# Performance work log

Hardware: AMD Instinct MI355X
Metric: run time of the kernel (lower is better)

## Reference

```python
import jax, jax.numpy as jnp
from jax import lax
import numpy as np

DIM = 256
D_INNER = 2 * DIM
STATE = 64
NUM_LAYERS = 2
NUM_STACKS = 4  # 0=h_fwd, 1=h_bwd, 2=v_fwd, 3=v_bwd
SPATIAL_H = 32
SPATIAL_W = 64
EPS = 1e-5


def setup_inputs() -> dict:
    key = jax.random.key(0)
    ks = jax.random.split(key, 24)
    w = lambda k, shape: jax.random.normal(k, shape, jnp.float32) * 0.02
    B = 4
    N = SPATIAL_H * SPATIAL_W
    inp = {
        "stream_sem": jax.random.normal(ks[0], (B, N, DIM), jnp.float32),
        "stream_inst": jax.random.normal(ks[1], (B, N, DIM), jnp.float32),
        # per-stack, per-layer Mamba params
        "Wx": w(ks[2], (NUM_STACKS, NUM_LAYERS, DIM, D_INNER)),
        "Wz": w(ks[3], (NUM_STACKS, NUM_LAYERS, DIM, D_INNER)),
        "Wdt": w(ks[4], (NUM_STACKS, NUM_LAYERS, DIM, D_INNER)),
        "WB": w(ks[5], (NUM_STACKS, NUM_LAYERS, DIM, STATE)),
        "WC": w(ks[6], (NUM_STACKS, NUM_LAYERS, DIM, STATE)),
        "A_log": jax.random.normal(ks[7], (NUM_STACKS, NUM_LAYERS, D_INNER), jnp.float32) * 0.1,
        "Dskip": jnp.ones((NUM_STACKS, NUM_LAYERS, D_INNER), jnp.float32),
        "dt_bias": w(ks[8], (NUM_STACKS, NUM_LAYERS, D_INNER)),
        "Wout": w(ks[9], (NUM_STACKS, NUM_LAYERS, D_INNER, DIM)),
        "ln_s": jnp.ones((NUM_STACKS, NUM_LAYERS, DIM), jnp.float32),
        "ln_b": jnp.zeros((NUM_STACKS, NUM_LAYERS, DIM), jnp.float32),
        # merge gates for the two DirectionalBiCMS (0=horizontal, 1=vertical)
        "gate_W": w(ks[10], (2, 2 * DIM, DIM)),
        "gate_b": jnp.zeros((2, DIM), jnp.float32),
        # final sem/inst merges (Linear + LayerNorm); 0=sem, 1=inst
        "merge_W": w(ks[11], (2, 2 * DIM, DIM)),
        "merge_b": jnp.zeros((2, DIM), jnp.float32),
        "merge_ln_s": jnp.ones((2, DIM), jnp.float32),
        "merge_ln_b": jnp.zeros((2, DIM), jnp.float32),
    }
    return inp


def _layernorm(x, s, b):
    mu = jnp.mean(x, axis=-1, keepdims=True)
    xc = x - mu
    var = jnp.mean(xc * xc, axis=-1, keepdims=True)
    return xc * lax.rsqrt(var + EPS) * s + b


def _mamba_layer(x, Wx, Wz, Wdt, WB, WC, A_log, Dskip, dt_bias, Wout, ln_s, ln_b):
    # x: (Bs, L, DIM)
    h = _layernorm(x, ln_s, ln_b)
    xin = h @ Wx                                   # (Bs, L, D_INNER)
    z = h @ Wz
    dt = jax.nn.softplus(h @ Wdt + dt_bias)        # (Bs, L, D_INNER)
    Bm = h @ WB                                    # (Bs, L, STATE)
    Cm = h @ WC
    xs = jax.nn.silu(xin)
    A = -jnp.exp(A_log)                            # (D_INNER,)

    def step(hs, ins):
        dt_t, x_t, B_t, C_t = ins                  # (Bs,Di),(Bs,Di),(Bs,S),(Bs,S)
        hs = jnp.exp(dt_t * A)[..., None] * hs + (dt_t * x_t)[..., None] * B_t[:, None, :]
        y = jnp.einsum('bds,bs->bd', hs, C_t)
        return hs, y

    Bsz = x.shape[0]
    h0 = jnp.zeros((Bsz, Wx.shape[1], WB.shape[1]), x.dtype)
    mv = lambda a: jnp.moveaxis(a, 1, 0)
    _, yT = lax.scan(step, h0, (mv(dt), mv(xs), mv(Bm), mv(Cm)))
    y = jnp.moveaxis(yT, 0, 1) + Dskip * xs
    return x + (y * jax.nn.silu(z)) @ Wout


def _stack(x, si, P):
    for l in range(P['Wx'].shape[1]):
        x = _mamba_layer(x, P['Wx'][si, l], P['Wz'][si, l], P['Wdt'][si, l],
                         P['WB'][si, l], P['WC'][si, l], P['A_log'][si, l],
                         P['Dskip'][si, l], P['dt_bias'][si, l], P['Wout'][si, l],
                         P['ln_s'][si, l], P['ln_b'][si, l])
    return x


def _bicms(a, b, si_fwd, si_bwd, gW, gb, P):
    # interleave: (Bs, 2L, D)
    Bs, L, D = a.shape
    inter = jnp.stack([a, b], axis=2).reshape(Bs, 2 * L, D)
    fwd = _stack(inter, si_fwd, P)
    bwd = jnp.flip(_stack(jnp.flip(inter, axis=1), si_bwd, P), axis=1)
    gate = jax.nn.sigmoid(jnp.concatenate([fwd, bwd], axis=-1) @ gW + gb)
    merged = gate * fwd + (1.0 - gate) * bwd
    return merged[:, 0::2], merged[:, 1::2]


def _forward(stream_sem, stream_inst, P):
    B, N, D = stream_sem.shape
    H, W = SPATIAL_H, SPATIAL_W
    sem_2d = stream_sem.reshape(B, H, W, D)
    inst_2d = stream_inst.reshape(B, H, W, D)

    # horizontal (row) scans
    h_sem, h_inst = _bicms(sem_2d.reshape(B * H, W, D), inst_2d.reshape(B * H, W, D),
                           0, 1, P['gate_W'][0], P['gate_b'][0], P)
    h_sem = h_sem.reshape(B, H, W, D)
    h_inst = h_inst.reshape(B, H, W, D)

    # vertical (column) scans
    sem_cols = jnp.transpose(sem_2d, (0, 2, 1, 3)).reshape(B * W, H, D)
    inst_cols = jnp.transpose(inst_2d, (0, 2, 1, 3)).reshape(B * W, H, D)
    v_sem, v_inst = _bicms(sem_cols, inst_cols, 2, 3, P['gate_W'][1], P['gate_b'][1], P)
    v_sem = jnp.transpose(v_sem.reshape(B, W, H, D), (0, 2, 1, 3))
    v_inst = jnp.transpose(v_inst.reshape(B, W, H, D), (0, 2, 1, 3))

    fused_sem = _layernorm(jnp.concatenate([h_sem, v_sem], -1) @ P['merge_W'][0] + P['merge_b'][0],
                           P['merge_ln_s'][0], P['merge_ln_b'][0]).reshape(B, N, D)
    fused_inst = _layernorm(jnp.concatenate([h_inst, v_inst], -1) @ P['merge_W'][1] + P['merge_b'][1],
                            P['merge_ln_s'][1], P['merge_ln_b'][1]).reshape(B, N, D)
    return fused_sem, fused_inst


def reference(stream_sem, stream_inst, Wx, Wz, Wdt, WB, WC, A_log, Dskip, dt_bias, Wout,
              ln_s, ln_b, gate_W, gate_b, merge_W, merge_b, merge_ln_s, merge_ln_b):
    P = dict(Wx=Wx, Wz=Wz, Wdt=Wdt, WB=WB, WC=WC, A_log=A_log, Dskip=Dskip,
             dt_bias=dt_bias, Wout=Wout, ln_s=ln_s, ln_b=ln_b, gate_W=gate_W,
             gate_b=gate_b, merge_W=merge_W, merge_b=merge_b,
             merge_ln_s=merge_ln_s, merge_ln_b=merge_ln_b)
    return _forward(stream_sem, stream_inst, P)
```

## Files before the change

### kernel.cpp

```cpp
#include <hip/hip_runtime.h>
#include <cstdint>

#define STATE  64
#define DINNER 512

typedef __bf16  bf16x8 __attribute__((ext_vector_type(8)));
typedef float   f32x4  __attribute__((ext_vector_type(4)));

static __device__ __forceinline__ float sigmoidf_(float x){ return 1.f/(1.f+expf(-x)); }
static __device__ __forceinline__ float siluf_(float x){ return x/(1.f+expf(-x)); }
static __device__ __forceinline__ float softplusf_(float x){
    return fmaxf(x,0.f) + log1pf(expf(-fabsf(x)));
}
static __device__ __forceinline__ unsigned short f2bf(float f){
    unsigned int u = __float_as_uint(f);
    unsigned int r = (u + 0x7FFFu + ((u>>16)&1u)) >> 16;
    return (unsigned short)r;
}
static __device__ __forceinline__ float b2f(unsigned short s){
    return __uint_as_float(((unsigned int)s)<<16);
}
static __device__ __forceinline__ void gload16(const void* g, void* l){
    __builtin_amdgcn_global_load_lds(
        (const __attribute__((address_space(1))) void*)g,
        (__attribute__((address_space(3))) void*)l, 16, 0, 0);
}

__global__ __launch_bounds__(64) void prep_k(const float* __restrict__ sem,
                                             const float* __restrict__ inst,
                                             float* __restrict__ xbuf, int bi)
{
    int u = blockIdx.x;
    int lane = threadIdx.x;
    int t; long n;
    if (bi == 0) {
        int s = u >> 7; t = u & 127;
        int b = s >> 5, r = s & 31; int w = t >> 1;
        n = (long)b*2048 + r*64 + w;
    } else {
        int s = u >> 6; t = u & 63;
        int b = s >> 6, w = s & 63; int hh = t >> 1;
        n = (long)b*2048 + hh*64 + w;
    }
    const float* src = ((t & 1) ? inst : sem) + n*256 + lane*4;
    float4 v = *(const float4*)src;
    *(float4*)(xbuf + (long)u*256 + lane*4) = v;
    *(float4*)(xbuf + ((long)16384 + u)*256 + lane*4) = v;
}

template<bool BF16OUT>
__global__ __launch_bounds__(64) void ln_k(const float* __restrict__ x,
                                           void* __restrict__ outp,
                                           const float* __restrict__ sp,
                                           const float* __restrict__ bp,
                                           int pStride, int tokensPerZ)
{
    long tok = blockIdx.x;
    int z = (int)(tok / tokensPerZ);
    const float* s = sp + (long)z*pStride;
    const float* b = bp + (long)z*pStride;
    int lane = threadIdx.x;
    float4 v = *(const float4*)(x + tok*256 + lane*4);
    float sum = v.x+v.y+v.z+v.w;
    #pragma unroll
    for (int o=32;o>=1;o>>=1) sum += __shfl_xor(sum,o);
    float mu = sum * (1.f/256.f);
    float cx=v.x-mu, cy=v.y-mu, cz=v.z-mu, cw=v.w-mu;
    float vs = cx*cx+cy*cy+cz*cz+cw*cw;
    #pragma unroll
    for (int o=32;o>=1;o>>=1) vs += __shfl_xor(vs,o);
    float r = rsqrtf(vs*(1.f/256.f) + 1e-5f);
    float4 sv = *(const float4*)(s + lane*4);
    float4 bv = *(const float4*)(b + lane*4);
    float o0 = cx*r*sv.x + bv.x;
    float o1 = cy*r*sv.y + bv.y;
    float o2 = cz*r*sv.z + bv.z;
    float o3 = cw*r*sv.w + bv.w;
    if (BF16OUT) {
        ushort4 o4; o4.x=f2bf(o0); o4.y=f2bf(o1); o4.z=f2bf(o2); o4.w=f2bf(o3);
        *(ushort4*)((unsigned short*)outp + tok*256 + lane*4) = o4;
    } else {
        float4 o4; o4.x=o0; o4.y=o1; o4.z=o2; o4.w=o3;
        *(float4*)((float*)outp + tok*256 + lane*4) = o4;
    }
}

__global__ __launch_bounds__(256) void tcvt_k(const float* __restrict__ src,
                                              unsigned short* __restrict__ dst,
                                              int K, int N, long sStride, long dStride,
                                              int dRowOff, int dLd)
{
    __shared__ float t[32][33];
    int z = blockIdx.z;
    int n0 = blockIdx.x<<5, k0 = blockIdx.y<<5;
    int tx = threadIdx.x & 31, ty = threadIdx.x >> 5;
    const float* s = src + (long)z*sStride;
    #pragma unroll
    for (int i=0;i<4;i++) t[ty+8*i][tx] = s[(long)(k0+ty+8*i)*N + n0+tx];
    __syncthreads();
    unsigned short* d = dst + (long)z*dStride;
    #pragma unroll
    for (int i=0;i<4;i++)
        d[(long)(dRowOff + n0 + ty + 8*i)*dLd + k0 + tx] = f2bf(t[tx][ty+8*i]);
}

enum { EPI_SILU=0, EPI_SOFTPLUS=1, EPI_PLAINF=2, EPI_RES=3, EPI_GATE=4, EPI_BIAS=5 };

template<int MODE>
__global__ __launch_bounds__(256) void mgemm_k(
    const unsigned short* __restrict__ A, long aZ, int lda,
    const unsigned short* __restrict__ W, long wZ,
    float* __restrict__ Cf, unsigned short* __restrict__ Cb,
    int M, int K, int N,
    const float* __restrict__ p1, long s1,
    const float* __restrict__ p2,
    const float* __restrict__ p3)
{
    __shared__ __align__(16) unsigned short As[2][2048];
    __shared__ __align__(16) unsigned short Bs[2][4096];
    int z = blockIdx.z;
    const unsigned short* Az = A + (long)z*aZ;
    const unsigned short* Wz = W + (long)z*wZ;
    int bm = blockIdx.x<<6, bn = blockIdx.y<<7;
    int tid = threadIdx.x, w = tid>>6, lane = tid&63;
    int wm = w>>1, wn = w&1;
    int l15 = lane&15, l4 = lane>>4;

    f32x4 acc[2][4];
    #pragma unroll
    for (int i=0;i<2;i++)
        #pragma unroll
        for (int j=0;j<4;j++)
            acc[i][j] = (f32x4){0.f,0.f,0.f,0.f};

    auto stage = [&](int buf, int koff) {
        gload16(Az + (long)(bm + (w<<4) + l15)*lda + koff + (l4<<3), &As[buf][w<<9]);
        #pragma unroll
        for (int r = 0; r < 2; ++r) {
            int g = (r<<2) + w;
            gload16(Wz + (long)(bn + (g<<4) + l15)*K + koff + (l4<<3), &Bs[buf][g<<9]);
        }
    };

    stage(0, 0);
    __syncthreads();
    int nk = K >> 5;
    for (int t = 0; t < nk; ++t) {
        int cur = t & 1;
        if (t + 1 < nk) stage(cur ^ 1, (t + 1) << 5);
        bf16x8 a[2], b[4];
        #pragma unroll
        for (int i=0;i<2;i++)
            a[i] = *(const bf16x8*)&As[cur][(((wm<<1)+i)<<9) + (lane<<3)];
        #pragma unroll
        for (int j=0;j<4;j++)
            b[j] = *(const bf16x8*)&Bs[cur][(((wn<<2)+j)<<9) + (lane<<3)];
        #pragma unroll
        for (int i=0;i<2;i++)
            #pragma unroll
            for (int j=0;j<4;j++)
                acc[i][j] = __builtin_amdgcn_mfma_f32_16x16x32_bf16(a[i], b[j], acc[i][j], 0, 0, 0);
        __syncthreads();
    }

    #pragma unroll
    for (int i=0;i<2;i++){
        int row0 = bm + (wm<<5) + (i<<4) + (l4<<2);
        #pragma unroll
        for (int j=0;j<4;j++){
            int col = bn + (wn<<6) + (j<<4) + l15;
            #pragma unroll
            for (int tt=0;tt<4;tt++){
                int row = row0 + tt;
                long rowz = (long)z*M + row;
                float v = acc[i][j][tt];
                if (MODE == EPI_SILU) {
                    Cb[rowz*(long)N + col] = f2bf(siluf_(v));
                } else if (MODE == EPI_SOFTPLUS) {
                    Cb[rowz*(long)N + col] = f2bf(softplusf_(v + p1[(long)z*s1 + col]));
                } else if (MODE == EPI_PLAINF) {
                    Cf[rowz*(long)N + col] = v;
                } else if (MODE == EPI_RES) {
                    long rc = rowz*256 + col;
                    float o = Cf[rc] + v;
                    Cf[rc] = o;
                    Cb[(long)row*512 + (z<<8) + col] = f2bf(o);
                } else if (MODE == EPI_GATE) {
                    float gg = sigmoidf_(v + p3[col]);
                    long rl = (long)row*256 + col;
                    Cb[rl] = f2bf(gg*p1[rl] + (1.f-gg)*p2[rl]);
                } else {
                    Cf[(long)row*256 + col] = v + p1[col];
                }
            }
        }
    }
}

__global__ __launch_bounds__(256) void scan_k(
    const unsigned short* __restrict__ dtq, const unsigned short* __restrict__ xs,
    unsigned short* zg,
    const float* __restrict__ BC,
    const float* __restrict__ Alog, long aStride,
    const float* __restrict__ Dsk,
    int Bs, int Lint)
{
    __shared__ __align__(16) float bcs[4][3][128];
    int q = blockIdx.x;
    int stack = (q >= Bs) ? 1 : 0;
    int seq = q - stack*Bs;
    int tid = threadIdx.x;
    int w = tid >> 6, lane = tid & 63;
    int dl = lane & 31;
    int sh = lane >> 5;
    int d = (blockIdx.y << 7) + (w << 5) + dl;
    float Ad  = -expf(Alog[(long)stack*aStride + d]);
    float dsk = Dsk[(long)stack*aStride + d];
    long base = (long)stack*16384 + (long)seq*Lint;
    long tok  = stack ? (base + Lint - 1) : base;
    long step = stack ? -1 : 1;

    float hs[32];
    #pragma unroll
    for (int s=0;s<32;s++) hs[s] = 0.f;

    long t1 = (Lint > 1) ? tok + step : tok;
    if (lane < 32) {
        gload16(BC + tok*128 + (lane<<2), &bcs[w][0][lane<<2]);
        gload16(BC + t1*128  + (lane<<2), &bcs[w][1][lane<<2]);
    }
    float dvA = b2f(dtq[tok*DINNER + d]);
    float xvA = b2f(xs [tok*DINNER + d]);
    float zvA = b2f(zg [tok*DINNER + d]);
    float dvB = b2f(dtq[t1*DINNER + d]);
    float xvB = b2f(xs [t1*DINNER + d]);
    float zvB = b2f(zg [t1*DINNER + d]);

    int so = sh << 5;
    int cur = 0;
    for (int it = 0; it < Lint; ++it) {
        int sb = cur + 2; if (sb >= 3) sb -= 3;
        long tok2 = (it + 2 < Lint) ? tok + 2*step : tok;
        if (lane < 32) gload16(BC + tok2*128 + (lane<<2), &bcs[w][sb][lane<<2]);
        float dvC = b2f(dtq[tok2*DINNER + d]);
        float xvC = b2f(xs [tok2*DINNER + d]);
        float zvC = b2f(zg [tok2*DINNER + d]);
        asm volatile("s_waitcnt vmcnt(10)" ::: "memory");
        __builtin_amdgcn_sched_barrier(0);

        float wdec = expf(dvA * Ad);
        float u = dvA * xvA;
        const float4* B4 = (const float4*)&bcs[w][cur][so];
        const float4* C4 = (const float4*)&bcs[w][cur][64 + so];
        float a0=0.f, a1=0.f, a2=0.f, a3=0.f;
        #pragma unroll
        for (int s4=0; s4<8; ++s4){
            float4 bv = B4[s4], cv = C4[s4];
            int s0 = s4<<2;
            hs[s0]   = fmaf(wdec, hs[s0],   u*bv.x); a0 = fmaf(hs[s0],   cv.x, a0);
            hs[s0+1] = fmaf(wdec, hs[s0+1], u*bv.y); a1 = fmaf(hs[s0+1], cv.y, a1);
            hs[s0+2] = fmaf(wdec, hs[s0+2], u*bv.z); a2 = fmaf(hs[s0+2], cv.z, a2);
            hs[s0+3] = fmaf(wdec, hs[s0+3], u*bv.w); a3 = fmaf(hs[s0+3], cv.w, a3);
        }
        float part = (a0+a1)+(a2+a3);
        float yv = part + __shfl_xor(part, 32);
        if (sh == 0)
            zg[tok*DINNER + d] = f2bf((yv + dsk*xvA) * zvA);

        dvA=dvB; xvA=xvB; zvA=zvB;
        dvB=dvC; xvB=xvC; zvB=zvC;
        tok += step;
        cur = cur + 1; if (cur == 3) cur = 0;
    }
}

__global__ __launch_bounds__(64) void gather_k(const unsigned short* __restrict__ mh,
                                               const unsigned short* __restrict__ mv,
                                               unsigned short* __restrict__ catsem,
                                               unsigned short* __restrict__ catinst)
{
    int n = blockIdx.x;
    int lane = threadIdx.x;
    int b = n >> 11;
    int rem = n & 2047;
    int r = rem >> 6, w = rem & 63;
    long hrow = ((long)(b*32 + r)*128 + 2*w)*256;
    long vrow = ((long)(b*64 + w)*64  + 2*r)*256;
    ushort4 hsv = *(const ushort4*)(mh + hrow + lane*4);
    ushort4 vsv = *(const ushort4*)(mv + vrow + lane*4);
    ushort4 hiv = *(const ushort4*)(mh + hrow + 256 + lane*4);
    ushort4 viv = *(const ushort4*)(mv + vrow + 256 + lane*4);
    *(ushort4*)(catsem  + (long)n*512 +       lane*4) = hsv;
    *(ushort4*)(catsem  + (long)n*512 + 256 + lane*4) = vsv;
    *(ushort4*)(catinst + (long)n*512 +       lane*4) = hiv;
    *(ushort4*)(catinst + (long)n*512 + 256 + lane*4) = viv;
}

extern "C" void kernel_launch(void* const* d_in, const int* in_sizes, int n_in,
                              void* d_out, int out_size, void* d_ws, size_t ws_size,
                              hipStream_t stream)
{
    (void)in_sizes; (void)n_in; (void)out_size; (void)ws_size;
    const float* sem  = (const float*)d_in[0];
    const float* inst = (const float*)d_in[1];
    const float* Wx   = (const float*)d_in[2];
    const float* Wz   = (const float*)d_in[3];
    const float* Wdt  = (const float*)d_in[4];
    const float* WB   = (const float*)d_in[5];
    const float* WC   = (const float*)d_in[6];
    const float* Alog = (const float*)d_in[7];
    const float* Dsk  = (const float*)d_in[8];
    const float* dtb  = (const float*)d_in[9];
    const float* Wo   = (const float*)d_in[10];
    const float* lns  = (const float*)d_in[11];
    const float* lnb  = (const float*)d_in[12];
    const float* gW   = (const float*)d_in[13];
    const float* gb   = (const float*)d_in[14];
    const float* mW   = (const float*)d_in[15];
    const float* mb   = (const float*)d_in[16];
    const float* mlns = (const float*)d_in[17];
    const float* mlnb = (const float*)d_in[18];
    float* out = (float*)d_out;

    char* base = (char*)d_ws;
    const long T2 = 32768;
    float* xbuf = (float*)base;                         base += T2*256*4;
    char* dtRegion = base;                              base += T2*512*4;
    unsigned short* xsb  = (unsigned short*)base;       base += T2*512*2;
    unsigned short* hb16 = (unsigned short*)base;       base += T2*256*2;
    unsigned short* gzb  = (unsigned short*)base;       base += T2*512*2;
    char* xbcRegion = base;                             base += T2*128*4;
    unsigned short* mh   = (unsigned short*)base;       base += (long)16384*256*2;
    unsigned short* mv   = (unsigned short*)base;       base += (long)16384*256*2;
    unsigned short* wxT  = (unsigned short*)base;       base += (long)8*512*256*2;
    unsigned short* wzT  = (unsigned short*)base;       base += (long)8*512*256*2;
    unsigned short* wdtT = (unsigned short*)base;       base += (long)8*512*256*2;
    unsigned short* woT  = (unsigned short*)base;       base += (long)8*256*512*2;
    unsigned short* wbc  = (unsigned short*)base;       base += (long)8*128*256*2;
    unsigned short* gwT  = (unsigned short*)base;       base += (long)2*256*512*2;
    unsigned short* mwT  = (unsigned short*)base;       base += (long)2*256*512*2;
    unsigned short* dt16 = (unsigned short*)dtRegion;
    float* logits = (float*)dtRegion;
    float* bcf = (float*)xbcRegion;
    unsigned short* xb16 = (unsigned short*)xbcRegion;
    unsigned short* cats = xsb;
    unsigned short* cati = xsb + (long)8192*512;

    dim3 t256(256);
    tcvt_k<<<dim3(16,8,8), t256, 0, stream>>>(Wx,  wxT, 256, 512, 131072L, 131072L, 0, 256);
    tcvt_k<<<dim3(16,8,8), t256, 0, stream>>>(Wz,  wzT, 256, 512, 131072L, 131072L, 0, 256);
    tcvt_k<<<dim3(16,8,8), t256, 0, stream>>>(Wdt, wdtT,256, 512, 131072L, 131072L, 0, 256);
    tcvt_k<<<dim3(8,16,8), t256, 0, stream>>>(Wo,  woT, 512, 256, 131072L, 131072L, 0, 512);
    tcvt_k<<<dim3(2,8,8),  t256, 0, stream>>>(WB,  wbc, 256, 64,  16384L,  32768L,  0, 256);
    tcvt_k<<<dim3(2,8,8),  t256, 0, stream>>>(WC,  wbc, 256, 64,  16384L,  32768L, 64, 256);
    tcvt_k<<<dim3(8,16,2), t256, 0, stream>>>(gW,  gwT, 512, 256, 131072L, 131072L, 0, 512);
    tcvt_k<<<dim3(8,16,2), t256, 0, stream>>>(mW,  mwT, 512, 256, 131072L, 131072L, 0, 512);

    for (int bi = 0; bi < 2; ++bi) {
        int Bs   = (bi == 0) ? 128 : 256;
        int Lint = (bi == 0) ? 128 : 64;
        prep_k<<<dim3(16384), dim3(64), 0, stream>>>(sem, inst, xbuf, bi);

        for (int l = 0; l < 2; ++l) {
            long slOff = (long)bi*4 + l;

            ln_k<true><<<dim3(32768), dim3(64), 0, stream>>>(
                xbuf, hb16, lns + slOff*256, lnb + slOff*256, 512, 16384);

            mgemm_k<EPI_SILU><<<dim3(256,4,2), t256, 0, stream>>>(
                hb16, 16384L*256, 256, wxT + slOff*131072, 262144L,
                nullptr, xsb, 16384, 256, 512,
                nullptr, 0L, nullptr, nullptr);

            mgemm_k<EPI_SILU><<<dim3(256,4,2), t256, 0, stream>>>(
                hb16, 16384L*256, 256, wzT + slOff*131072, 262144L,
                nullptr, gzb, 16384, 256, 512,
                nullptr, 0L, nullptr, nullptr);

            mgemm_k<EPI_SOFTPLUS><<<dim3(256,4,2), t256, 0, stream>>>(
                hb16, 16384L*256, 256, wdtT + slOff*131072, 262144L,
                nullptr, dt16, 16384, 256, 512,
                dtb + slOff*512, 1024L, nullptr, nullptr);

            mgemm_k<EPI_PLAINF><<<dim3(256,1,2), t256, 0, stream>>>(
                hb16, 16384L*256, 256, wbc + slOff*32768, 65536L,
                bcf, nullptr, 16384, 256, 128,
                nullptr, 0L, nullptr, nullptr);

            scan_k<<<dim3(2*Bs,4), t256, 0, stream>>>(
                dt16, xsb, gzb, bcf, Alog + slOff*512, 1024L,
                Dsk + slOff*512, Bs, Lint);

            mgemm_k<EPI_RES><<<dim3(256,2,2), t256, 0, stream>>>(
                gzb, 16384L*512, 512, woT + slOff*131072, 262144L,
                xbuf, xb16, 16384, 512, 256,
                nullptr, 0L, nullptr, nullptr);
        }

        mgemm_k<EPI_GATE><<<dim3(256,2,1), t256, 0, stream>>>(
            xb16, 0L, 512, gwT + (long)bi*131072, 0L,
            nullptr, (bi ? mv : mh), 16384, 512, 256,
            xbuf, 0L, xbuf + (long)16384*256, gb + bi*256);
    }

    gather_k<<<dim3(8192), dim3(64), 0, stream>>>(mh, mv, cats, cati);
    for (int mi = 0; mi < 2; ++mi) {
        const unsigned short* cat = (mi == 0) ? cats : cati;
        mgemm_k<EPI_BIAS><<<dim3(128,2,1), t256, 0, stream>>>(
            cat, 0L, 512, mwT + (long)mi*131072, 0L,
            logits, nullptr, 8192, 512, 256,
            mb + mi*256, 0L, nullptr, nullptr);
        ln_k<false><<<dim3(8192), dim3(64), 0, stream>>>(
            logits, out + (long)mi*2097152, mlns + mi*256, mlnb + mi*256, 0, 8192);
    }
}
```

Before: 1.329 ms.

## Process two channels per thread in scan kernel to reuse B/C loads

Each thread in the selective scan now handles two inner channels (d and d+32), so each shared-memory B/C read feeds twice the recurrence work. The grid's y dimension is halved to match. The decay exponential also switches to exp2f with a pre-scaled log2(e) constant. The cost is twice the state registers per thread and half as many blocks, which lowers parallelism and occupancy in a latency-bound sequential scan. The vmcnt wait threshold is raised to match the larger number of loads in flight.

Result: slower. 1.361 ms (+2.4%).

```diff
diff --git a/kernel.cpp b/kernel.cpp
--- a/kernel.cpp
+++ b/kernel.cpp
@@ -213,28 +213,30 @@
     int w = tid >> 6, lane = tid & 63;
     int dl = lane & 31;
     int sh = lane >> 5;
-    int d = (blockIdx.y << 7) + (w << 5) + dl;
-    float Ad  = -expf(Alog[(long)stack*aStride + d]);
-    float dsk = Dsk[(long)stack*aStride + d];
+    int d0 = (blockIdx.y << 8) + (w << 6) + dl;
+    int d1 = d0 + 32;
+    const float L2E = 1.44269504088896340736f;
+    float Ad0  = -expf(Alog[(long)stack*aStride + d0]) * L2E;
+    float Ad1  = -expf(Alog[(long)stack*aStride + d1]) * L2E;
+    float dsk0 = Dsk[(long)stack*aStride + d0];
+    float dsk1 = Dsk[(long)stack*aStride + d1];
     long base = (long)stack*16384 + (long)seq*Lint;
     long tok  = stack ? (base + Lint - 1) : base;
     long step = stack ? -1 : 1;
 
-    float hs[32];
-    #pragma unroll
-    for (int s=0;s<32;s++) hs[s] = 0.f;
+    float hs0[32], hs1[32];
+    #pragma unroll
+    for (int s=0;s<32;s++) { hs0[s] = 0.f; hs1[s] = 0.f; }
 
     long t1 = (Lint > 1) ? tok + step : tok;
     if (lane < 32) {
         gload16(BC + tok*128 + (lane<<2), &bcs[w][0][lane<<2]);
         gload16(BC + t1*128  + (lane<<2), &bcs[w][1][lane<<2]);
     }
-    float dvA = b2f(dtq[tok*DINNER + d]);
-    float xvA = b2f(xs [tok*DINNER + d]);
-    float zvA = b2f(zg [tok*DINNER + d]);
-    float dvB = b2f(dtq[t1*DINNER + d]);
-    float xvB = b2f(xs [t1*DINNER + d]);
-    float zvB = b2f(zg [t1*DINNER + d]);
+    float dvA0 = b2f(dtq[tok*DINNER + d0]), xvA0 = b2f(xs[tok*DINNER + d0]), zvA0 = b2f(zg[tok*DINNER + d0]);
+    float dvA1 = b2f(dtq[tok*DINNER + d1]), xvA1 = b2f(xs[tok*DINNER + d1]), zvA1 = b2f(zg[tok*DINNER + d1]);
+    float dvB0 = b2f(dtq[t1*DINNER + d0]),  xvB0 = b2f(xs[t1*DINNER + d0]),  zvB0 = b2f(zg[t1*DINNER + d0]);
+    float dvB1 = b2f(dtq[t1*DINNER + d1]),  xvB1 = b2f(xs[t1*DINNER + d1]),  zvB1 = b2f(zg[t1*DINNER + d1]);
 
     int so = sh << 5;
     int cur = 0;
@@ -242,33 +244,46 @@
         int sb = cur + 2; if (sb >= 3) sb -= 3;
         long tok2 = (it + 2 < Lint) ? tok + 2*step : tok;
         if (lane < 32) gload16(BC + tok2*128 + (lane<<2), &bcs[w][sb][lane<<2]);
-        float dvC = b2f(dtq[tok2*DINNER + d]);
-        float xvC = b2f(xs [tok2*DINNER + d]);
-        float zvC = b2f(zg [tok2*DINNER + d]);
-        asm volatile("s_waitcnt vmcnt(10)" ::: "memory");
+        float dvC0 = b2f(dtq[tok2*DINNER + d0]);
+        float xvC0 = b2f(xs [tok2*DINNER + d0]);
+        float zvC0 = b2f(zg [tok2*DINNER + d0]);
+        float dvC1 = b2f(dtq[tok2*DINNER + d1]);
+        float xvC1 = b2f(xs [tok2*DINNER + d1]);
+        float zvC1 = b2f(zg [tok2*DINNER + d1]);
+        asm volatile("s_waitcnt vmcnt(18)" ::: "memory");
         __builtin_amdgcn_sched_barrier(0);
 
-        float wdec = expf(dvA * Ad);
-        float u = dvA * xvA;
+        float w0 = exp2f(dvA0 * Ad0);
+        float w1 = exp2f(dvA1 * Ad1);
+        float u0 = dvA0 * xvA0;
+        float u1 = dvA1 * xvA1;
         const float4* B4 = (const float4*)&bcs[w][cur][so];
         const float4* C4 = (const float4*)&bcs[w][cur][64 + so];
-        float a0=0.f, a1=0.f, a2=0.f, a3=0.f;
+        float p00=0.f, p01=0.f, p10=0.f, p11=0.f;
         #pragma unroll
         for (int s4=0; s4<8; ++s4){
             float4 bv = B4[s4], cv = C4[s4];
             int s0 = s4<<2;
-            hs[s0]   = fmaf(wdec, hs[s0],   u*bv.x); a0 = fmaf(hs[s0],   cv.x, a0);
-            hs[s0+1] = fmaf(wdec, hs[s0+1], u*bv.y); a1 = fmaf(hs[s0+1], cv.y, a1);
-            hs[s0+2] = fmaf(wdec, hs[s0+2], u*bv.z); a2 = fmaf(hs[s0+2], cv.z, a2);
-            hs[s0+3] = fmaf(wdec, hs[s0+3], u*bv.w); a3 = fmaf(hs[s0+3], cv.w, a3);
+            hs0[s0]   = fmaf(w0, hs0[s0],   u0*bv.x); p00 = fmaf(hs0[s0],   cv.x, p00);
+            hs0[s0+1] = fmaf(w0, hs0[s0+1], u0*bv.y); p01 = fmaf(hs0[s0+1], cv.y, p01);
+            hs0[s0+2] = fmaf(w0, hs0[s0+2], u0*bv.z); p00 = fmaf(hs0[s0+2], cv.z, p00);
+            hs0[s0+3] = fmaf(w0, hs0[s0+3], u0*bv.w); p01 = fmaf(hs0[s0+3], cv.w, p01);
+            hs1[s0]   = fmaf(w1, hs1[s0],   u1*bv.x); p10 = fmaf(hs1[s0],   cv.x, p10);
+            hs1[s0+1] = fmaf(w1, hs1[s0+1], u1*bv.y); p11 = fmaf(hs1[s0+1], cv.y, p11);
+            hs1[s0+2] = fmaf(w1, hs1[s0+2], u1*bv.z); p10 = fmaf(hs1[s0+2], cv.z, p10);
+            hs1[s0+3] = fmaf(w1, hs1[s0+3], u1*bv.w); p11 = fmaf(hs1[s0+3], cv.w, p11);
         }
-        float part = (a0+a1)+(a2+a3);
-        float yv = part + __shfl_xor(part, 32);
-        if (sh == 0)
-            zg[tok*DINNER + d] = f2bf((yv + dsk*xvA) * zvA);
-
-        dvA=dvB; xvA=xvB; zvA=zvB;
-        dvB=dvC; xvB=xvC; zvB=zvC;
+        float part0 = p00 + p01;
+        float part1 = p10 + p11;
+        float yv0 = part0 + __shfl_xor(part0, 32);
+        float yv1 = part1 + __shfl_xor(part1, 32);
+        if (sh == 0) {
+            zg[tok*DINNER + d0] = f2bf((yv0 + dsk0*xvA0) * zvA0);
+            zg[tok*DINNER + d1] = f2bf((yv1 + dsk1*xvA1) * zvA1);
+        }
+
+        dvA0=dvB0; xvA0=xvB0; zvA0=zvB0;  dvA1=dvB1; xvA1=xvB1; zvA1=zvB1;
+        dvB0=dvC0; xvB0=xvC0; zvB0=zvC0;  dvB1=dvC1; xvB1=xvC1; zvB1=zvC1;
         tok += step;
         cur = cur + 1; if (cur == 3) cur = 0;
     }
@@ -387,7 +402,7 @@
                 bcf, nullptr, 16384, 256, 128,
                 nullptr, 0L, nullptr, nullptr);
 
-            scan_k<<<dim3(2*Bs,4), t256, 0, stream>>>(
+            scan_k<<<dim3(2*Bs,2), t256, 0, stream>>>(
                 dt16, xsb, gzb, bcf, Alog + slOff*512, 1024L,
                 Dsk + slOff*512, Bs, Lint);
 
```
